# Performance work log

Hardware: AMD Instinct MI355X
Metric: run time of the kernel (lower is better)

Reference implementation:

```python
import jax, jax.numpy as jnp
import numpy as np

H = W = 56; WS = 7; SHIFT = 3; NH = 6; DIM = 192; DEPTH = 2
HD = DIM // NH; NW = (H // WS) * (W // WS); N = WS * WS; SCALE = HD ** -0.5

# relative position index (constant, as in WindowAttention.__init__)
_c = np.stack(np.meshgrid(np.arange(WS), np.arange(WS), indexing='ij')).reshape(2, -1)
_r = (_c[:, :, None] - _c[:, None, :]).transpose(1, 2, 0)
_r[..., 0] += WS - 1; _r[..., 1] += WS - 1; _r[..., 0] *= 2 * WS - 1
RPI = jnp.asarray(_r.sum(-1).reshape(-1))  # (N*N,)

def _build_mask():
    # shifted-window attention mask (constant, built in SwinTransformerBlock.__init__)
    img = np.zeros((H, W))
    sl = (slice(0, -WS), slice(-WS, -SHIFT), slice(-SHIFT, None))
    cnt = 0
    for hs in sl:
        for ws_ in sl:
            img[hs, ws_] = cnt; cnt += 1
    mw = img.reshape(H // WS, WS, W // WS, WS).transpose(0, 2, 1, 3).reshape(-1, N)
    am = mw[:, None, :] - mw[:, :, None]  # (nW, N, N)
    return jnp.asarray(np.where(am != 0, -100.0, 0.0).astype(np.float32))

MASK = _build_mask()

def _ln(x, g, b):
    m = jnp.mean(x, -1, keepdims=True)
    v = jnp.mean((x - m) ** 2, -1, keepdims=True)
    return (x - m) * jax.lax.rsqrt(v + 1e-5) * g + b

def setup_inputs() -> dict:
    key = jax.random.key(0)
    ks = jax.random.split(key, 8)
    B = 64; s = 0.02
    return {
        'x': jax.random.normal(ks[0], (B, H * W, DIM), jnp.float32),
        'norm1_g': jnp.ones((DEPTH, DIM), jnp.float32),
        'norm1_b': jnp.zeros((DEPTH, DIM), jnp.float32),
        'qkv_w': jax.random.normal(ks[1], (DEPTH, DIM, 3 * DIM), jnp.float32) * s,
        'qkv_b': jnp.zeros((DEPTH, 3 * DIM), jnp.float32),
        'rpb': jax.random.normal(ks[2], (DEPTH, (2 * WS - 1) ** 2, NH), jnp.float32) * s,
        'proj_w': jax.random.normal(ks[3], (DEPTH, DIM, DIM), jnp.float32) * s,
        'proj_b': jnp.zeros((DEPTH, DIM), jnp.float32),
        'norm2_g': jnp.ones((DEPTH, DIM), jnp.float32),
        'norm2_b': jnp.zeros((DEPTH, DIM), jnp.float32),
        'fc1_w': jax.random.normal(ks[4], (DEPTH, DIM, 4 * DIM), jnp.float32) * s,
        'fc1_b': jnp.zeros((DEPTH, 4 * DIM), jnp.float32),
        'fc2_w': jax.random.normal(ks[5], (DEPTH, 4 * DIM, DIM), jnp.float32) * s,
        'fc2_b': jnp.zeros((DEPTH, DIM), jnp.float32),
    }

def reference(x, norm1_g, norm1_b, qkv_w, qkv_b, rpb, proj_w, proj_b,
              norm2_g, norm2_b, fc1_w, fc1_b, fc2_w, fc2_b):
    B = x.shape[0]
    for i in range(DEPTH):
        shift = 0 if i % 2 == 0 else WS // 2
        # --- windowed MHSA branch ---
        h = _ln(x, norm1_g[i], norm1_b[i]).reshape(B, H, W, DIM)
        if shift:
            h = jnp.roll(h, (-shift, -shift), (1, 2))
        # window partition -> (B*nW, N, C)
        w = h.reshape(B, H // WS, WS, W // WS, WS, DIM)
        w = w.transpose(0, 1, 3, 2, 4, 5).reshape(B * NW, N, DIM)
        qkv = (w @ qkv_w[i] + qkv_b[i]).reshape(B * NW, N, 3, NH, HD)
        qkv = qkv.transpose(2, 0, 3, 1, 4)  # (3, Bw, NH, N, HD)
        q, k, v = qkv[0] * SCALE, qkv[1], qkv[2]
        attn = jnp.einsum('bhnd,bhmd->bhnm', q, k)  # (Bw, NH, N, N)
        bias = rpb[i][RPI].reshape(N, N, NH).transpose(2, 0, 1)
        attn = attn + bias[None]
        if shift:
            attn = attn.reshape(B, NW, NH, N, N) + MASK[None, :, None]
            attn = attn.reshape(B * NW, NH, N, N)
        attn = jax.nn.softmax(attn, axis=-1)
        o = jnp.einsum('bhnm,bhmd->bhnd', attn, v)
        o = o.transpose(0, 2, 1, 3).reshape(B * NW, N, DIM)
        o = o @ proj_w[i] + proj_b[i]
        # window reverse
        h = o.reshape(B, H // WS, W // WS, WS, WS, DIM)
        h = h.transpose(0, 1, 3, 2, 4, 5).reshape(B, H, W, DIM)
        if shift:
            h = jnp.roll(h, (shift, shift), (1, 2))
        x = x + h.reshape(B, H * W, DIM)
        # --- MLP branch ---
        m = _ln(x, norm2_g[i], norm2_b[i])
        m = jax.nn.gelu(m @ fc1_w[i] + fc1_b[i], approximate=False)
        x = x + (m @ fc2_w[i] + fc2_b[i])
    return x
```

## Files before the change

### kernel.cpp

```cpp
#include <hip/hip_runtime.h>
#include <stdint.h>

#define MROWS  200704
#define SCALE_ 0.17677669529663687f

typedef __attribute__((ext_vector_type(8))) short bf16x8;
typedef __attribute__((ext_vector_type(4))) float f32x4;
union V8 { uint4 u; unsigned short s[8]; };

__device__ __forceinline__ float bf2f(unsigned short u) {
  union { unsigned int i; float f; } c; c.i = ((unsigned int)u) << 16; return c.f;
}
__device__ __forceinline__ unsigned short f2bf(float f) {
  union { float f; unsigned int i; } c; c.f = f;
  unsigned int lsb = (c.i >> 16) & 1;
  return (unsigned short)((c.i + 0x7fffu + lsb) >> 16);
}
__device__ __forceinline__ float gelu_f(float x) {
  float x2 = x * x;
  float arg = x * fmaf(0.07135481f, x2, 1.59576912f);
  float e = __expf(arg);
  float r = __builtin_amdgcn_rcpf(1.0f + e);
  return fmaf(-x, r, x);
}

__global__ __launch_bounds__(256) void wt_k(const float* __restrict__ W,
    unsigned short* __restrict__ Wt, int K, int N)
{
  int idx = blockIdx.x * 256 + threadIdx.x;
  if (idx < K * N) {
    int k = idx / N, n = idx - k * N;
    Wt[(size_t)n * K + k] = f2bf(W[idx]);
  }
}

__global__ __launch_bounds__(256) void ln_k(const float* __restrict__ X,
    const float* __restrict__ g, const float* __restrict__ b,
    unsigned short* __restrict__ out, int shift)
{
  int wr = blockIdx.x * 4 + (threadIdx.x >> 6);
  int lane = threadIdx.x & 63;
  int win = wr / 49, n = wr % 49;
  int bi = win >> 6, w64 = win & 63;
  int wh = w64 >> 3, ww = w64 & 7;
  int ti = n / 7, tj = n % 7;
  int gh = wh * 7 + ti + shift; if (gh >= 56) gh -= 56;
  int gw = ww * 7 + tj + shift; if (gw >= 56) gw -= 56;
  size_t srow = (size_t)bi * 3136 + gh * 56 + gw;
  const float* xr = X + srow * 192;
  float v0 = xr[lane], v1 = xr[lane + 64], v2 = xr[lane + 128];
  float s  = v0 + v1 + v2;
  float s2 = v0*v0 + v1*v1 + v2*v2;
  #pragma unroll
  for (int m = 32; m >= 1; m >>= 1) { s += __shfl_xor(s, m); s2 += __shfl_xor(s2, m); }
  float mean = s * (1.0f/192.0f);
  float var  = s2 * (1.0f/192.0f) - mean*mean;
  float inv  = rsqrtf(var + 1e-5f);
  unsigned short* orow = out + (size_t)wr * 192;
  orow[lane]       = f2bf((v0-mean)*inv*g[lane]      + b[lane]);
  orow[lane+64]    = f2bf((v1-mean)*inv*g[lane+64]   + b[lane+64]);
  orow[lane+128]   = f2bf((v2-mean)*inv*g[lane+128]  + b[lane+128]);
}

template<int EPI>
__global__ __launch_bounds__(256, 4) void gemm2_k(
    const unsigned short* __restrict__ A,
    const unsigned short* __restrict__ Wt,
    const float* __restrict__ bias,
    unsigned short* __restrict__ Cbf,
    const float* __restrict__ Xres,
    float* __restrict__ Xdst,
    int N, int shift)
{
  __shared__ unsigned short As[128][40];
  const int tid = threadIdx.x;
  const int lane = tid & 63, wv = tid >> 6;
  const int wm = wv >> 1, wn = wv & 1;
  const int row0 = blockIdx.x * 128;
  const int n0   = blockIdx.y * 64;
  const int fr = lane & 15, kq = (lane >> 4) * 8;
  bf16x8 bfr[6][2];
  #pragma unroll
  for (int ks = 0; ks < 6; ++ks)
    #pragma unroll
    for (int ni = 0; ni < 2; ++ni)
      bfr[ks][ni] = *reinterpret_cast<const bf16x8*>(
          &Wt[(size_t)(n0 + wn*32 + ni*16 + fr) * 192 + ks*32 + kq]);
  const int sr  = tid >> 1, ssg = (tid & 1) * 16;
  const unsigned short* arow = A + (size_t)(row0 + sr) * 192 + ssg;
  uint4 a0 = *reinterpret_cast<const uint4*>(arow);
  uint4 a1 = *reinterpret_cast<const uint4*>(arow + 8);
  f32x4 acc[4][2] = {};
  #pragma unroll
  for (int ks = 0; ks < 6; ++ks) {
    __syncthreads();
    *reinterpret_cast<uint4*>(&As[sr][ssg])     = a0;
    *reinterpret_cast<uint4*>(&As[sr][ssg + 8]) = a1;
    if (ks < 5) {
      a0 = *reinterpret_cast<const uint4*>(arow + (ks+1)*32);
      a1 = *reinterpret_cast<const uint4*>(arow + (ks+1)*32 + 8);
    }
    __syncthreads();
    #pragma unroll
    for (int mi = 0; mi < 4; ++mi) {
      bf16x8 afr = *reinterpret_cast<const bf16x8*>(&As[wm*64 + mi*16 + fr][kq]);
      #pragma unroll
      for (int ni = 0; ni < 2; ++ni)
        acc[mi][ni] = __builtin_amdgcn_mfma_f32_16x16x32_bf16(afr, bfr[ks][ni], acc[mi][ni], 0, 0, 0);
    }
  }
  const int lcol = lane & 15, lr4 = (lane >> 4) * 4;
  #pragma unroll
  for (int mi = 0; mi < 4; ++mi)
  #pragma unroll
  for (int ni = 0; ni < 2; ++ni)
  #pragma unroll
  for (int i = 0; i < 4; ++i) {
    int gr = row0 + wm*64 + mi*16 + lr4 + i;
    int gc = n0 + wn*32 + ni*16 + lcol;
    float v = acc[mi][ni][i] + bias[gc];
    if (EPI == 0) {
      Cbf[(size_t)gr * N + gc] = f2bf(v);
    } else {
      int win = gr / 49, n = gr % 49;
      int bi = win >> 6, w64 = win & 63;
      int wh = w64 >> 3, ww = w64 & 7;
      int ti = n / 7, tj = n % 7;
      int gh = wh*7 + ti + shift; if (gh >= 56) gh -= 56;
      int gw = ww*7 + tj + shift; if (gw >= 56) gw -= 56;
      size_t idx = ((size_t)bi * 3136 + gh * 56 + gw) * 192 + gc;
      Xdst[idx] = Xres[idx] + v;
    }
  }
}

__global__ __launch_bounds__(512, 4) void mlp_k(
    const float* __restrict__ X,
    const float* __restrict__ g, const float* __restrict__ b,
    const unsigned short* __restrict__ W1t,
    const float* __restrict__ b1,
    const unsigned short* __restrict__ W2t,
    const float* __restrict__ b2,
    float* __restrict__ Y)
{
  __shared__ unsigned short As[64][200];
  __shared__ unsigned short Hs[64][396];
  const int row0 = blockIdx.x * 64;
  const int tid = threadIdx.x, lane = tid & 63, wv = tid >> 6;
  #pragma unroll
  for (int r = 0; r < 8; ++r) {
    int row = wv * 8 + r;
    const float* xr = X + (size_t)(row0 + row) * 192;
    float v0 = xr[lane], v1 = xr[lane + 64], v2 = xr[lane + 128];
    float s  = v0 + v1 + v2;
    float s2 = v0*v0 + v1*v1 + v2*v2;
    #pragma unroll
    for (int m = 32; m >= 1; m >>= 1) { s += __shfl_xor(s, m); s2 += __shfl_xor(s2, m); }
    float mean = s * (1.0f/192.0f);
    float var  = s2 * (1.0f/192.0f) - mean*mean;
    float inv  = rsqrtf(var + 1e-5f);
    As[row][lane]       = f2bf((v0-mean)*inv*g[lane]      + b[lane]);
    As[row][lane+64]    = f2bf((v1-mean)*inv*g[lane+64]   + b[lane+64]);
    As[row][lane+128]   = f2bf((v2-mean)*inv*g[lane+128]  + b[lane+128]);
  }
  __syncthreads();
  const int fr = lane & 15, kq = (lane >> 4) * 8;
  const int lcol = lane & 15, lr4 = (lane >> 4) * 4;
  const int wm2 = wv >> 2, wn2 = wv & 3;
  f32x4 acc2[2][3] = {};
  for (int hh = 0; hh < 2; ++hh) {
    f32x4 acc1[4][3] = {};
    const int c0 = hh * 384 + wv * 48;
    #pragma unroll
    for (int k0 = 0; k0 < 192; k0 += 32) {
      bf16x8 bfr[3];
      #pragma unroll
      for (int ni = 0; ni < 3; ++ni)
        bfr[ni] = *reinterpret_cast<const bf16x8*>(&W1t[(size_t)(c0 + ni*16 + fr) * 192 + k0 + kq]);
      #pragma unroll
      for (int mi = 0; mi < 4; ++mi) {
        bf16x8 afr = *reinterpret_cast<const bf16x8*>(&As[mi*16 + fr][k0 + kq]);
        #pragma unroll
        for (int ni = 0; ni < 3; ++ni)
          acc1[mi][ni] = __builtin_amdgcn_mfma_f32_16x16x32_bf16(afr, bfr[ni], acc1[mi][ni], 0, 0, 0);
      }
    }
    __syncthreads();
    #pragma unroll
    for (int mi = 0; mi < 4; ++mi)
    #pragma unroll
    for (int ni = 0; ni < 3; ++ni)
    #pragma unroll
    for (int i = 0; i < 4; ++i) {
      int rr = mi*16 + lr4 + i;
      int cc = wv*48 + ni*16 + lcol;
      float v = acc1[mi][ni][i] + b1[hh*384 + cc];
      Hs[rr][cc] = f2bf(gelu_f(v));
    }
    __syncthreads();
    #pragma unroll
    for (int k0 = 0; k0 < 384; k0 += 32) {
      bf16x8 bfr[3];
      #pragma unroll
      for (int ni = 0; ni < 3; ++ni)
        bfr[ni] = *reinterpret_cast<const bf16x8*>(
            &W2t[(size_t)(wn2*48 + ni*16 + fr) * 768 + hh*384 + k0 + kq]);
      #pragma unroll
      for (int mi = 0; mi < 2; ++mi) {
        bf16x8 afr = *reinterpret_cast<const bf16x8*>(&Hs[wm2*32 + mi*16 + fr][k0 + kq]);
        #pragma unroll
        for (int ni = 0; ni < 3; ++ni)
          acc2[mi][ni] = __builtin_amdgcn_mfma_f32_16x16x32_bf16(afr, bfr[ni], acc2[mi][ni], 0, 0, 0);
      }
    }
  }
  #pragma unroll
  for (int mi = 0; mi < 2; ++mi)
  #pragma unroll
  for (int ni = 0; ni < 3; ++ni)
  #pragma unroll
  for (int i = 0; i < 4; ++i) {
    int grow = row0 + wm2*32 + mi*16 + lr4 + i;
    int gc = wn2*48 + ni*16 + lcol;
    float v = acc2[mi][ni][i] + b2[gc];
    size_t idx = (size_t)grow * 192 + gc;
    Y[idx] = X[idx] + v;
  }
}

template<bool SHIFTED>
__global__ __launch_bounds__(64) void attn_k(
    const unsigned short* __restrict__ qkv,
    const float* __restrict__ rpb,
    unsigned short* __restrict__ out)
{
  __shared__ float kv[2][49][32];
  int blk = blockIdx.x;
  int win = blk / 6, h = blk - win * 6;
  int lane = threadIdx.x;
  const unsigned short* base = qkv + (size_t)win * 49 * 576;
  for (int idx = lane; idx < 196; idx += 64) {
    int n = idx >> 2, sg = (idx & 3) * 8;
    V8 kk, vv;
    kk.u = *reinterpret_cast<const uint4*>(base + n*576 + 192 + h*32 + sg);
    vv.u = *reinterpret_cast<const uint4*>(base + n*576 + 384 + h*32 + sg);
    #pragma unroll
    for (int j = 0; j < 8; ++j) { kv[0][n][sg+j] = bf2f(kk.s[j]); kv[1][n][sg+j] = bf2f(vv.s[j]); }
  }
  __syncthreads();
  if (lane < 49) {
    float q[32];
    const unsigned short* qr = base + (size_t)lane * 576 + h * 32;
    #pragma unroll
    for (int sg = 0; sg < 4; ++sg) {
      V8 qq; qq.u = *reinterpret_cast<const uint4*>(qr + sg*8);
      #pragma unroll
      for (int j = 0; j < 8; ++j) q[sg*8+j] = bf2f(qq.s[j]) * SCALE_;
    }
    int ti = lane / 7, tj = lane - ti * 7;
    int wi = win & 63, wh = wi >> 3, ww = wi & 7;
    int rid = 0;
    if (SHIFTED) {
      int hh = wh*7 + ti, wg = ww*7 + tj;
      rid = (hh < 49 ? 0 : (hh < 53 ? 1 : 2)) * 3 + (wg < 49 ? 0 : (wg < 53 ? 1 : 2));
    }
    float s[49];
    float mx = -1e30f;
    #pragma unroll
    for (int m = 0; m < 49; ++m) {
      float a = 0.f;
      #pragma unroll
      for (int d4 = 0; d4 < 8; ++d4) {
        float4 kf = *reinterpret_cast<const float4*>(&kv[0][m][d4*4]);
        a += q[d4*4+0]*kf.x + q[d4*4+1]*kf.y + q[d4*4+2]*kf.z + q[d4*4+3]*kf.w;
      }
      int mi = m / 7, mj = m - mi * 7;
      a += rpb[((ti - mi + 6) * 13 + (tj - mj + 6)) * 6 + h];
      if (SHIFTED) {
        int hh = wh*7 + mi, wg = ww*7 + mj;
        int rid2 = (hh < 49 ? 0 : (hh < 53 ? 1 : 2)) * 3 + (wg < 49 ? 0 : (wg < 53 ? 1 : 2));
        if (rid2 != rid) a -= 100.f;
      }
      s[m] = a;
      mx = fmaxf(mx, a);
    }
    float sum = 0.f;
    #pragma unroll
    for (int m = 0; m < 49; ++m) { float e = __expf(s[m] - mx); s[m] = e; sum += e; }
    float rs = 1.f / sum;
    float o[32];
    #pragma unroll
    for (int d = 0; d < 32; ++d) o[d] = 0.f;
    #pragma unroll
    for (int m = 0; m < 49; ++m) {
      float p = s[m] * rs;
      #pragma unroll
      for (int d4 = 0; d4 < 8; ++d4) {
        float4 vf = *reinterpret_cast<const float4*>(&kv[1][m][d4*4]);
        o[d4*4+0] += p*vf.x; o[d4*4+1] += p*vf.y; o[d4*4+2] += p*vf.z; o[d4*4+3] += p*vf.w;
      }
    }
    unsigned short* orow = out + ((size_t)win * 49 + lane) * 192 + h * 32;
    #pragma unroll
    for (int sg = 0; sg < 4; ++sg) {
      V8 pk;
      #pragma unroll
      for (int j = 0; j < 8; ++j) pk.s[j] = f2bf(o[sg*8+j]);
      *reinterpret_cast<uint4*>(orow + sg*8) = pk.u;
    }
  }
}

extern "C" void kernel_launch(void* const* d_in, const int* in_sizes, int n_in,
                              void* d_out, int out_size, void* d_ws, size_t ws_size,
                              hipStream_t stream) {
  const float* x    = (const float*)d_in[0];
  const float* n1g  = (const float*)d_in[1];
  const float* n1b  = (const float*)d_in[2];
  const float* qkvw = (const float*)d_in[3];
  const float* qkvb = (const float*)d_in[4];
  const float* rpb  = (const float*)d_in[5];
  const float* pw   = (const float*)d_in[6];
  const float* pb   = (const float*)d_in[7];
  const float* n2g  = (const float*)d_in[8];
  const float* n2b  = (const float*)d_in[9];
  const float* f1w  = (const float*)d_in[10];
  const float* f1b  = (const float*)d_in[11];
  const float* f2w  = (const float*)d_in[12];
  const float* f2b  = (const float*)d_in[13];
  float* out = (float*)d_out;

  const size_t XBYTES = (size_t)MROWS * 192 * 4;
  const size_t ABYTES = (size_t)MROWS * 192 * 2;
  const size_t QBYTES = (size_t)MROWS * 576 * 2;
  char* ws = (char*)d_ws;
  float* x1 = (float*)ws;
  unsigned short* Abuf = (unsigned short*)(ws + XBYTES);
  unsigned short* Bbuf = (unsigned short*)(ws + XBYTES + ABYTES);
  unsigned short* WT   = (unsigned short*)(ws + XBYTES + ABYTES + QBYTES);
  const size_t WQ = 110592, WP = 36864, W1 = 147456, W2 = 147456;
  const size_t WD = WQ + WP + W1 + W2;

  for (int d = 0; d < 2; ++d) {
    unsigned short* wt = WT + d * WD;
    wt_k<<<(int)((WQ + 255)/256), 256, 0, stream>>>(qkvw + (size_t)d*WQ, wt,                 192, 576);
    wt_k<<<(int)((WP + 255)/256), 256, 0, stream>>>(pw   + (size_t)d*WP, wt + WQ,            192, 192);
    wt_k<<<(int)((W1 + 255)/256), 256, 0, stream>>>(f1w  + (size_t)d*W1, wt + WQ + WP,       192, 768);
    wt_k<<<(int)((W2 + 255)/256), 256, 0, stream>>>(f2w  + (size_t)d*W2, wt + WQ + WP + W1,  768, 192);
  }

  const int LNBLK = MROWS / 4;
  const dim3 G_QKV(MROWS/128, 9), G_P(MROWS/128, 3);

  for (int i = 0; i < 2; ++i) {
    int shift = i ? 3 : 0;
    const float* xin = i ? (const float*)x1 : x;
    float* xfin = i ? out : x1;
    const unsigned short* wt = WT + i * WD;
    ln_k<<<LNBLK, 256, 0, stream>>>(xin, n1g + i*192, n1b + i*192, Abuf, shift);
    gemm2_k<0><<<G_QKV, 256, 0, stream>>>(Abuf, wt, qkvb + i*576, Bbuf, nullptr, nullptr, 576, 0);
    if (shift) attn_k<true ><<<4096*6, 64, 0, stream>>>(Bbuf, rpb + i*169*6, Abuf);
    else       attn_k<false><<<4096*6, 64, 0, stream>>>(Bbuf, rpb + i*169*6, Abuf);
    gemm2_k<1><<<G_P, 256, 0, stream>>>(Abuf, wt + WQ, pb + i*192, nullptr, xin, x1, 192, shift);
    mlp_k<<<MROWS/64, 512, 0, stream>>>(x1, n2g + i*192, n2b + i*192,
                                        wt + WQ + WP, f1b + i*768,
                                        wt + WQ + WP + W1, f2b + i*192, xfin);
  }
}
```

Before: 1.828 ms.

## Chunk MLP hidden dim into quarters to shrink LDS; swap GEMM grid axes

The fused MLP kernel now processes the 768-wide hidden layer in four 192-column chunks instead of two 384-column halves. Each wave computes a 32x48 tile per chunk rather than a 64x48 tile, which shrinks the hidden-activation LDS buffer by about half and the fc1 accumulators from 12 to 6. The launch bound rises from 4 to 6 blocks per CU to use the freed resources. Separately, the QKV and projection GEMM grids swap axes so adjacent blocks share the same row tile across column tiles, which should improve L2 reuse of A. The cost is twice as many sync/GELU-store phases per block and tighter register limits.

```diff
diff --git a/kernel.cpp b/kernel.cpp
--- a/kernel.cpp
+++ b/kernel.cpp
@@ -76,8 +76,8 @@
   const int tid = threadIdx.x;
   const int lane = tid & 63, wv = tid >> 6;
   const int wm = wv >> 1, wn = wv & 1;
-  const int row0 = blockIdx.x * 128;
-  const int n0   = blockIdx.y * 64;
+  const int row0 = blockIdx.y * 128;
+  const int n0   = blockIdx.x * 64;
   const int fr = lane & 15, kq = (lane >> 4) * 8;
   bf16x8 bfr[6][2];
   #pragma unroll
@@ -134,7 +134,7 @@
   }
 }
 
-__global__ __launch_bounds__(512, 4) void mlp_k(
+__global__ __launch_bounds__(512, 6) void mlp_k(
     const float* __restrict__ X,
     const float* __restrict__ g, const float* __restrict__ b,
     const unsigned short* __restrict__ W1t,
@@ -144,7 +144,7 @@
     float* __restrict__ Y)
 {
   __shared__ unsigned short As[64][200];
-  __shared__ unsigned short Hs[64][396];
+  __shared__ unsigned short Hs[64][200];
   const int row0 = blockIdx.x * 64;
   const int tid = threadIdx.x, lane = tid & 63, wv = tid >> 6;
   #pragma unroll
@@ -166,20 +166,20 @@
   __syncthreads();
   const int fr = lane & 15, kq = (lane >> 4) * 8;
   const int lcol = lane & 15, lr4 = (lane >> 4) * 4;
-  const int wm2 = wv >> 2, wn2 = wv & 3;
+  const int wm = wv >> 2, wn = wv & 3;
   f32x4 acc2[2][3] = {};
-  for (int hh = 0; hh < 2; ++hh) {
-    f32x4 acc1[4][3] = {};
-    const int c0 = hh * 384 + wv * 48;
-    #pragma unroll
-    for (int k0 = 0; k0 < 192; k0 += 32) {
+  for (int q = 0; q < 4; ++q) {
+    f32x4 acc1[2][3] = {};
+    #pragma unroll
+    for (int ks = 0; ks < 6; ++ks) {
       bf16x8 bfr[3];
       #pragma unroll
       for (int ni = 0; ni < 3; ++ni)
-        bfr[ni] = *reinterpret_cast<const bf16x8*>(&W1t[(size_t)(c0 + ni*16 + fr) * 192 + k0 + kq]);
-      #pragma unroll
-      for (int mi = 0; mi < 4; ++mi) {
-        bf16x8 afr = *reinterpret_cast<const bf16x8*>(&As[mi*16 + fr][k0 + kq]);
+        bfr[ni] = *reinterpret_cast<const bf16x8*>(
+            &W1t[(size_t)(q*192 + wn*48 + ni*16 + fr) * 192 + ks*32 + kq]);
+      #pragma unroll
+      for (int mi = 0; mi < 2; ++mi) {
+        bf16x8 afr = *reinterpret_cast<const bf16x8*>(&As[wm*32 + mi*16 + fr][ks*32 + kq]);
         #pragma unroll
         for (int ni = 0; ni < 3; ++ni)
           acc1[mi][ni] = __builtin_amdgcn_mfma_f32_16x16x32_bf16(afr, bfr[ni], acc1[mi][ni], 0, 0, 0);
@@ -187,27 +187,27 @@
     }
     __syncthreads();
     #pragma unroll
-    for (int mi = 0; mi < 4; ++mi)
+    for (int mi = 0; mi < 2; ++mi)
     #pragma unroll
     for (int ni = 0; ni < 3; ++ni)
     #pragma unroll
     for (int i = 0; i < 4; ++i) {
-      int rr = mi*16 + lr4 + i;
-      int cc = wv*48 + ni*16 + lcol;
-      float v = acc1[mi][ni][i] + b1[hh*384 + cc];
+      int rr = wm*32 + mi*16 + lr4 + i;
+      int cc = wn*48 + ni*16 + lcol;
+      float v = acc1[mi][ni][i] + b1[q*192 + cc];
       Hs[rr][cc] = f2bf(gelu_f(v));
     }
     __syncthreads();
     #pragma unroll
-    for (int k0 = 0; k0 < 384; k0 += 32) {
+    for (int ks = 0; ks < 6; ++ks) {
       bf16x8 bfr[3];
       #pragma unroll
       for (int ni = 0; ni < 3; ++ni)
         bfr[ni] = *reinterpret_cast<const bf16x8*>(
-            &W2t[(size_t)(wn2*48 + ni*16 + fr) * 768 + hh*384 + k0 + kq]);
+            &W2t[(size_t)(wn*48 + ni*16 + fr) * 768 + q*192 + ks*32 + kq]);
       #pragma unroll
       for (int mi = 0; mi < 2; ++mi) {
-        bf16x8 afr = *reinterpret_cast<const bf16x8*>(&Hs[wm2*32 + mi*16 + fr][k0 + kq]);
+        bf16x8 afr = *reinterpret_cast<const bf16x8*>(&Hs[wm*32 + mi*16 + fr][ks*32 + kq]);
         #pragma unroll
         for (int ni = 0; ni < 3; ++ni)
           acc2[mi][ni] = __builtin_amdgcn_mfma_f32_16x16x32_bf16(afr, bfr[ni], acc2[mi][ni], 0, 0, 0);
@@ -220,8 +220,8 @@
   for (int ni = 0; ni < 3; ++ni)
   #pragma unroll
   for (int i = 0; i < 4; ++i) {
-    int grow = row0 + wm2*32 + mi*16 + lr4 + i;
-    int gc = wn2*48 + ni*16 + lcol;
+    int grow = row0 + wm*32 + mi*16 + lr4 + i;
+    int gc = wn*48 + ni*16 + lcol;
     float v = acc2[mi][ni][i] + b2[gc];
     size_t idx = (size_t)grow * 192 + gc;
     Y[idx] = X[idx] + v;
@@ -350,7 +350,7 @@
   }
 
   const int LNBLK = MROWS / 4;
-  const dim3 G_QKV(MROWS/128, 9), G_P(MROWS/128, 3);
+  const dim3 G_QKV(9, MROWS/128), G_P(3, MROWS/128);
 
   for (int i = 0; i < 2; ++i) {
     int shift = i ? 3 : 0;
```

Measured after the change: 2.012 ms. +10.0%, slower.

## Fuse LayerNorm1 into the QKV GEMM, keeping normalized rows in LDS

Applied to the files above, without the earlier changes.

The separate LayerNorm kernel and QKV GEMM are merged into one kernel. Each block normalizes 128 gathered (shifted) rows straight into shared memory, then loops over all 9 output column tiles, reloading weight fragments for each tile. This removes the bf16 write and re-read of the normalized activations and one launch per depth. In exchange there are fewer blocks (no grid over N), a large LDS tile that limits occupancy, and serialized weight loads inside each block.

```diff
diff --git a/kernel.cpp b/kernel.cpp
--- a/kernel.cpp
+++ b/kernel.cpp
@@ -34,43 +34,79 @@
   }
 }
 
-__global__ __launch_bounds__(256) void ln_k(const float* __restrict__ X,
+__global__ __launch_bounds__(256, 3) void qkvf_k(const float* __restrict__ X,
     const float* __restrict__ g, const float* __restrict__ b,
-    unsigned short* __restrict__ out, int shift)
+    const unsigned short* __restrict__ Wt,
+    const float* __restrict__ bias,
+    unsigned short* __restrict__ C, int shift)
 {
-  int wr = blockIdx.x * 4 + (threadIdx.x >> 6);
-  int lane = threadIdx.x & 63;
-  int win = wr / 49, n = wr % 49;
-  int bi = win >> 6, w64 = win & 63;
-  int wh = w64 >> 3, ww = w64 & 7;
-  int ti = n / 7, tj = n % 7;
-  int gh = wh * 7 + ti + shift; if (gh >= 56) gh -= 56;
-  int gw = ww * 7 + tj + shift; if (gw >= 56) gw -= 56;
-  size_t srow = (size_t)bi * 3136 + gh * 56 + gw;
-  const float* xr = X + srow * 192;
-  float v0 = xr[lane], v1 = xr[lane + 64], v2 = xr[lane + 128];
-  float s  = v0 + v1 + v2;
-  float s2 = v0*v0 + v1*v1 + v2*v2;
-  #pragma unroll
-  for (int m = 32; m >= 1; m >>= 1) { s += __shfl_xor(s, m); s2 += __shfl_xor(s2, m); }
-  float mean = s * (1.0f/192.0f);
-  float var  = s2 * (1.0f/192.0f) - mean*mean;
-  float inv  = rsqrtf(var + 1e-5f);
-  unsigned short* orow = out + (size_t)wr * 192;
-  orow[lane]       = f2bf((v0-mean)*inv*g[lane]      + b[lane]);
-  orow[lane+64]    = f2bf((v1-mean)*inv*g[lane+64]   + b[lane+64]);
-  orow[lane+128]   = f2bf((v2-mean)*inv*g[lane+128]  + b[lane+128]);
-}
-
-template<int EPI>
-__global__ __launch_bounds__(256, 4) void gemm2_k(
+  __shared__ unsigned short As[128][200];
+  const int tid = threadIdx.x, lane = tid & 63, wv = tid >> 6;
+  const int row0 = blockIdx.x * 128;
+  #pragma unroll 2
+  for (int r = 0; r < 32; ++r) {
+    int row = wv * 32 + r, wr = row0 + row;
+    int win = wr / 49, n = wr - win * 49;
+    int bi = win >> 6, w64 = win & 63, wh = w64 >> 3, ww = w64 & 7;
+    int ti = n / 7, tj = n - ti * 7;
+    int gh = wh*7 + ti + shift; if (gh >= 56) gh -= 56;
+    int gw = ww*7 + tj + shift; if (gw >= 56) gw -= 56;
+    const float* xr = X + ((size_t)bi*3136 + gh*56 + gw) * 192;
+    float v0 = xr[lane], v1 = xr[lane + 64], v2 = xr[lane + 128];
+    float s  = v0 + v1 + v2;
+    float s2 = v0*v0 + v1*v1 + v2*v2;
+    #pragma unroll
+    for (int m = 32; m >= 1; m >>= 1) { s += __shfl_xor(s, m); s2 += __shfl_xor(s2, m); }
+    float mean = s * (1.0f/192.0f);
+    float var  = s2 * (1.0f/192.0f) - mean*mean;
+    float inv  = rsqrtf(var + 1e-5f);
+    As[row][lane]     = f2bf((v0-mean)*inv*g[lane]      + b[lane]);
+    As[row][lane+64]  = f2bf((v1-mean)*inv*g[lane+64]   + b[lane+64]);
+    As[row][lane+128] = f2bf((v2-mean)*inv*g[lane+128]  + b[lane+128]);
+  }
+  __syncthreads();
+  const int wm = wv >> 1, wn = wv & 1;
+  const int fr = lane & 15, kq = (lane >> 4) * 8;
+  const int lr4 = (lane >> 4) * 4;
+  #pragma unroll 1
+  for (int p = 0; p < 9; ++p) {
+    bf16x8 bfr[6][2];
+    #pragma unroll
+    for (int ks = 0; ks < 6; ++ks)
+      #pragma unroll
+      for (int ni = 0; ni < 2; ++ni)
+        bfr[ks][ni] = *reinterpret_cast<const bf16x8*>(
+            &Wt[(size_t)(p*64 + wn*32 + ni*16 + fr) * 192 + ks*32 + kq]);
+    f32x4 acc[4][2] = {};
+    #pragma unroll
+    for (int ks = 0; ks < 6; ++ks)
+      #pragma unroll
+      for (int mi = 0; mi < 4; ++mi) {
+        bf16x8 afr = *reinterpret_cast<const bf16x8*>(&As[wm*64 + mi*16 + fr][ks*32 + kq]);
+        #pragma unroll
+        for (int ni = 0; ni < 2; ++ni)
+          acc[mi][ni] = __builtin_amdgcn_mfma_f32_16x16x32_bf16(afr, bfr[ks][ni], acc[mi][ni], 0, 0, 0);
+      }
+    #pragma unroll
+    for (int mi = 0; mi < 4; ++mi)
+    #pragma unroll
+    for (int ni = 0; ni < 2; ++ni)
+    #pragma unroll
+    for (int i = 0; i < 4; ++i) {
+      int gr = row0 + wm*64 + mi*16 + lr4 + i;
+      int gc = p*64 + wn*32 + ni*16 + fr;
+      C[(size_t)gr * 576 + gc] = f2bf(acc[mi][ni][i] + bias[gc]);
+    }
+  }
+}
+
+__global__ __launch_bounds__(256, 4) void proj_k(
     const unsigned short* __restrict__ A,
     const unsigned short* __restrict__ Wt,
     const float* __restrict__ bias,
-    unsigned short* __restrict__ Cbf,
     const float* __restrict__ Xres,
     float* __restrict__ Xdst,
-    int N, int shift)
+    int shift)
 {
   __shared__ unsigned short As[128][40];
   const int tid = threadIdx.x;
@@ -119,18 +155,14 @@
     int gr = row0 + wm*64 + mi*16 + lr4 + i;
     int gc = n0 + wn*32 + ni*16 + lcol;
     float v = acc[mi][ni][i] + bias[gc];
-    if (EPI == 0) {
-      Cbf[(size_t)gr * N + gc] = f2bf(v);
-    } else {
-      int win = gr / 49, n = gr % 49;
-      int bi = win >> 6, w64 = win & 63;
-      int wh = w64 >> 3, ww = w64 & 7;
-      int ti = n / 7, tj = n % 7;
-      int gh = wh*7 + ti + shift; if (gh >= 56) gh -= 56;
-      int gw = ww*7 + tj + shift; if (gw >= 56) gw -= 56;
-      size_t idx = ((size_t)bi * 3136 + gh * 56 + gw) * 192 + gc;
-      Xdst[idx] = Xres[idx] + v;
-    }
+    int win = gr / 49, n = gr % 49;
+    int bi = win >> 6, w64 = win & 63;
+    int wh = w64 >> 3, ww = w64 & 7;
+    int ti = n / 7, tj = n % 7;
+    int gh = wh*7 + ti + shift; if (gh >= 56) gh -= 56;
+    int gw = ww*7 + tj + shift; if (gw >= 56) gw -= 56;
+    size_t idx = ((size_t)bi * 3136 + gh * 56 + gw) * 192 + gc;
+    Xdst[idx] = Xres[idx] + v;
   }
 }
 
@@ -349,19 +381,18 @@
     wt_k<<<(int)((W2 + 255)/256), 256, 0, stream>>>(f2w  + (size_t)d*W2, wt + WQ + WP + W1,  768, 192);
   }
 
-  const int LNBLK = MROWS / 4;
-  const dim3 G_QKV(MROWS/128, 9), G_P(MROWS/128, 3);
+  const dim3 G_P(MROWS/128, 3);
 
   for (int i = 0; i < 2; ++i) {
     int shift = i ? 3 : 0;
     const float* xin = i ? (const float*)x1 : x;
     float* xfin = i ? out : x1;
     const unsigned short* wt = WT + i * WD;
-    ln_k<<<LNBLK, 256, 0, stream>>>(xin, n1g + i*192, n1b + i*192, Abuf, shift);
-    gemm2_k<0><<<G_QKV, 256, 0, stream>>>(Abuf, wt, qkvb + i*576, Bbuf, nullptr, nullptr, 576, 0);
+    qkvf_k<<<MROWS/128, 256, 0, stream>>>(xin, n1g + i*192, n1b + i*192, wt,
+                                          qkvb + i*576, Bbuf, shift);
     if (shift) attn_k<true ><<<4096*6, 64, 0, stream>>>(Bbuf, rpb + i*169*6, Abuf);
     else       attn_k<false><<<4096*6, 64, 0, stream>>>(Bbuf, rpb + i*169*6, Abuf);
-    gemm2_k<1><<<G_P, 256, 0, stream>>>(Abuf, wt + WQ, pb + i*192, nullptr, xin, x1, 192, shift);
+    proj_k<<<G_P, 256, 0, stream>>>(Abuf, wt + WQ, pb + i*192, xin, x1, shift);
     mlp_k<<<MROWS/64, 512, 0, stream>>>(x1, n2g + i*192, n2b + i*192,
                                         wt + WQ + WP, f1b + i*768,
                                         wt + WQ + WP + W1, f2b + i*192, xfin);
```

Measured after the change: 1.837 ms. About the same (+0.5%).

## Fuse weight prep launches and restructure attention into single-pass bf16 LDS kernel

Applied to the files above, without the earlier changes.

Replaces the eight per-weight transpose/convert launches with one combined kernel over both depths. The attention kernel now packs four (window, head) groups per 256-thread block and stores K/V in shared memory as padded bf16 instead of fp32. It also fuses QK, exp and PV into one loop with no max subtraction, dropping the 49-element score array to cut register pressure and LDS footprint. Skipping the max subtraction relies on scores staying small (masked entries near -100), which risks overflow for larger logits.

```diff
diff --git a/kernel.cpp b/kernel.cpp
--- a/kernel.cpp
+++ b/kernel.cpp
@@ -3,6 +3,11 @@
 
 #define MROWS  200704
 #define SCALE_ 0.17677669529663687f
+#define WQ 110592
+#define WP 36864
+#define W1 147456
+#define W2 147456
+#define WD (WQ + WP + W1 + W2)
 
 typedef __attribute__((ext_vector_type(8))) short bf16x8;
 typedef __attribute__((ext_vector_type(4))) float f32x4;
@@ -24,13 +29,33 @@
   return fmaf(-x, r, x);
 }
 
-__global__ __launch_bounds__(256) void wt_k(const float* __restrict__ W,
-    unsigned short* __restrict__ Wt, int K, int N)
-{
-  int idx = blockIdx.x * 256 + threadIdx.x;
-  if (idx < K * N) {
-    int k = idx / N, n = idx - k * N;
-    Wt[(size_t)n * K + k] = f2bf(W[idx]);
+__global__ __launch_bounds__(256) void wtall_k(const float* __restrict__ qkvw,
+    const float* __restrict__ pw, const float* __restrict__ f1w,
+    const float* __restrict__ f2w, unsigned short* __restrict__ WT)
+{
+  int d = blockIdx.y;
+  int j = blockIdx.x * 256 + threadIdx.x;
+  if (j >= WD) return;
+  unsigned short* wt = WT + (size_t)d * WD;
+  if (j < WQ) {
+    const float* W = qkvw + (size_t)d * WQ;
+    int k = j / 576, n = j - k * 576;
+    wt[n * 192 + k] = f2bf(W[j]);
+  } else if (j < WQ + WP) {
+    int j2 = j - WQ;
+    const float* W = pw + (size_t)d * WP;
+    int k = j2 / 192, n = j2 - k * 192;
+    (wt + WQ)[n * 192 + k] = f2bf(W[j2]);
+  } else if (j < WQ + WP + W1) {
+    int j2 = j - WQ - WP;
+    const float* W = f1w + (size_t)d * W1;
+    int k = j2 / 768, n = j2 - k * 768;
+    (wt + WQ + WP)[n * 192 + k] = f2bf(W[j2]);
+  } else {
+    int j2 = j - WQ - WP - W1;
+    const float* W = f2w + (size_t)d * W2;
+    int k = j2 / 192, n = j2 - k * 192;
+    (wt + WQ + WP + W1)[(size_t)n * 768 + k] = f2bf(W[j2]);
   }
 }
 
@@ -229,23 +254,22 @@
 }
 
 template<bool SHIFTED>
-__global__ __launch_bounds__(64) void attn_k(
+__global__ __launch_bounds__(256) void attn_k(
     const unsigned short* __restrict__ qkv,
     const float* __restrict__ rpb,
     unsigned short* __restrict__ out)
 {
-  __shared__ float kv[2][49][32];
-  int blk = blockIdx.x;
-  int win = blk / 6, h = blk - win * 6;
-  int lane = threadIdx.x;
+  __shared__ unsigned short kvs[4][2][49][40];
+  const int tid = threadIdx.x, lane = tid & 63, wv = tid >> 6;
+  const int g = blockIdx.x * 4 + wv;
+  const int win = g / 6, h = g - win * 6;
   const unsigned short* base = qkv + (size_t)win * 49 * 576;
   for (int idx = lane; idx < 196; idx += 64) {
     int n = idx >> 2, sg = (idx & 3) * 8;
-    V8 kk, vv;
-    kk.u = *reinterpret_cast<const uint4*>(base + n*576 + 192 + h*32 + sg);
-    vv.u = *reinterpret_cast<const uint4*>(base + n*576 + 384 + h*32 + sg);
-    #pragma unroll
-    for (int j = 0; j < 8; ++j) { kv[0][n][sg+j] = bf2f(kk.s[j]); kv[1][n][sg+j] = bf2f(vv.s[j]); }
+    uint4 kk = *reinterpret_cast<const uint4*>(base + n*576 + 192 + h*32 + sg);
+    uint4 vv = *reinterpret_cast<const uint4*>(base + n*576 + 384 + h*32 + sg);
+    *reinterpret_cast<uint4*>(&kvs[wv][0][n][sg]) = kk;
+    *reinterpret_cast<uint4*>(&kvs[wv][1][n][sg]) = vv;
   }
   __syncthreads();
   if (lane < 49) {
@@ -264,48 +288,50 @@
       int hh = wh*7 + ti, wg = ww*7 + tj;
       rid = (hh < 49 ? 0 : (hh < 53 ? 1 : 2)) * 3 + (wg < 49 ? 0 : (wg < 53 ? 1 : 2));
     }
-    float s[49];
-    float mx = -1e30f;
-    #pragma unroll
+    float o[32];
+    #pragma unroll
+    for (int d = 0; d < 32; ++d) o[d] = 0.f;
+    float sum = 0.f;
+    #pragma unroll 1
     for (int m = 0; m < 49; ++m) {
-      float a = 0.f;
-      #pragma unroll
-      for (int d4 = 0; d4 < 8; ++d4) {
-        float4 kf = *reinterpret_cast<const float4*>(&kv[0][m][d4*4]);
-        a += q[d4*4+0]*kf.x + q[d4*4+1]*kf.y + q[d4*4+2]*kf.z + q[d4*4+3]*kf.w;
+      float a0 = 0.f, a1 = 0.f, a2 = 0.f, a3 = 0.f;
+      #pragma unroll
+      for (int d8 = 0; d8 < 4; ++d8) {
+        bf16x8 kf = *reinterpret_cast<const bf16x8*>(&kvs[wv][0][m][d8*8]);
+        a0 = fmaf(q[d8*8+0], bf2f((unsigned short)kf[0]), a0);
+        a1 = fmaf(q[d8*8+1], bf2f((unsigned short)kf[1]), a1);
+        a2 = fmaf(q[d8*8+2], bf2f((unsigned short)kf[2]), a2);
+        a3 = fmaf(q[d8*8+3], bf2f((unsigned short)kf[3]), a3);
+        a0 = fmaf(q[d8*8+4], bf2f((unsigned short)kf[4]), a0);
+        a1 = fmaf(q[d8*8+5], bf2f((unsigned short)kf[5]), a1);
+        a2 = fmaf(q[d8*8+6], bf2f((unsigned short)kf[6]), a2);
+        a3 = fmaf(q[d8*8+7], bf2f((unsigned short)kf[7]), a3);
       }
       int mi = m / 7, mj = m - mi * 7;
-      a += rpb[((ti - mi + 6) * 13 + (tj - mj + 6)) * 6 + h];
+      float a = (a0 + a1) + (a2 + a3)
+              + rpb[((ti - mi + 6) * 13 + (tj - mj + 6)) * 6 + h];
       if (SHIFTED) {
         int hh = wh*7 + mi, wg = ww*7 + mj;
         int rid2 = (hh < 49 ? 0 : (hh < 53 ? 1 : 2)) * 3 + (wg < 49 ? 0 : (wg < 53 ? 1 : 2));
         if (rid2 != rid) a -= 100.f;
       }
-      s[m] = a;
-      mx = fmaxf(mx, a);
-    }
-    float sum = 0.f;
-    #pragma unroll
-    for (int m = 0; m < 49; ++m) { float e = __expf(s[m] - mx); s[m] = e; sum += e; }
+      float e = __expf(a);
+      sum += e;
+      #pragma unroll
+      for (int d8 = 0; d8 < 4; ++d8) {
+        bf16x8 vf = *reinterpret_cast<const bf16x8*>(&kvs[wv][1][m][d8*8]);
+        #pragma unroll
+        for (int j = 0; j < 8; ++j)
+          o[d8*8+j] = fmaf(e, bf2f((unsigned short)vf[j]), o[d8*8+j]);
+      }
+    }
     float rs = 1.f / sum;
-    float o[32];
-    #pragma unroll
-    for (int d = 0; d < 32; ++d) o[d] = 0.f;
-    #pragma unroll
-    for (int m = 0; m < 49; ++m) {
-      float p = s[m] * rs;
-      #pragma unroll
-      for (int d4 = 0; d4 < 8; ++d4) {
-        float4 vf = *reinterpret_cast<const float4*>(&kv[1][m][d4*4]);
-        o[d4*4+0] += p*vf.x; o[d4*4+1] += p*vf.y; o[d4*4+2] += p*vf.z; o[d4*4+3] += p*vf.w;
-      }
-    }
     unsigned short* orow = out + ((size_t)win * 49 + lane) * 192 + h * 32;
     #pragma unroll
     for (int sg = 0; sg < 4; ++sg) {
       V8 pk;
       #pragma unroll
-      for (int j = 0; j < 8; ++j) pk.s[j] = f2bf(o[sg*8+j]);
+      for (int j = 0; j < 8; ++j) pk.s[j] = f2bf(o[sg*8+j] * rs);
       *reinterpret_cast<uint4*>(orow + sg*8) = pk.u;
     }
   }
@@ -338,16 +364,8 @@
   unsigned short* Abuf = (unsigned short*)(ws + XBYTES);
   unsigned short* Bbuf = (unsigned short*)(ws + XBYTES + ABYTES);
   unsigned short* WT   = (unsigned short*)(ws + XBYTES + ABYTES + QBYTES);
-  const size_t WQ = 110592, WP = 36864, W1 = 147456, W2 = 147456;
-  const size_t WD = WQ + WP + W1 + W2;
-
-  for (int d = 0; d < 2; ++d) {
-    unsigned short* wt = WT + d * WD;
-    wt_k<<<(int)((WQ + 255)/256), 256, 0, stream>>>(qkvw + (size_t)d*WQ, wt,                 192, 576);
-    wt_k<<<(int)((WP + 255)/256), 256, 0, stream>>>(pw   + (size_t)d*WP, wt + WQ,            192, 192);
-    wt_k<<<(int)((W1 + 255)/256), 256, 0, stream>>>(f1w  + (size_t)d*W1, wt + WQ + WP,       192, 768);
-    wt_k<<<(int)((W2 + 255)/256), 256, 0, stream>>>(f2w  + (size_t)d*W2, wt + WQ + WP + W1,  768, 192);
-  }
+
+  wtall_k<<<dim3((WD + 255)/256, 2), 256, 0, stream>>>(qkvw, pw, f1w, f2w, WT);
 
   const int LNBLK = MROWS / 4;
   const dim3 G_QKV(MROWS/128, 9), G_P(MROWS/128, 3);
@@ -356,11 +374,11 @@
     int shift = i ? 3 : 0;
     const float* xin = i ? (const float*)x1 : x;
     float* xfin = i ? out : x1;
-    const unsigned short* wt = WT + i * WD;
+    const unsigned short* wt = WT + (size_t)i * WD;
     ln_k<<<LNBLK, 256, 0, stream>>>(xin, n1g + i*192, n1b + i*192, Abuf, shift);
     gemm2_k<0><<<G_QKV, 256, 0, stream>>>(Abuf, wt, qkvb + i*576, Bbuf, nullptr, nullptr, 576, 0);
-    if (shift) attn_k<true ><<<4096*6, 64, 0, stream>>>(Bbuf, rpb + i*169*6, Abuf);
-    else       attn_k<false><<<4096*6, 64, 0, stream>>>(Bbuf, rpb + i*169*6, Abuf);
+    if (shift) attn_k<true ><<<4096*6/4, 256, 0, stream>>>(Bbuf, rpb + i*169*6, Abuf);
+    else       attn_k<false><<<4096*6/4, 256, 0, stream>>>(Bbuf, rpb + i*169*6, Abuf);
     gemm2_k<1><<<G_P, 256, 0, stream>>>(Abuf, wt + WQ, pb + i*192, nullptr, xin, x1, 192, shift);
     mlp_k<<<MROWS/64, 512, 0, stream>>>(x1, n2g + i*192, n2b + i*192,
                                         wt + WQ + WP, f1b + i*768,
```

Result: slower. 1.945 ms (+6.4%).
